# Kernel optimization log

Measured on AMD Instinct MI355X. Metric: run time of the kernel, lower is better.

Reference implementation:

```python
import jax, jax.numpy as jnp
import numpy as np

# module hyperparameters (match init_kwargs)
IN_PLANES = 64
OUT = 64            # out_planes
N_HASHES = 4
CHUNK = 25          # chunk_size
GROUPS = 8
KS = 56             # kernel_size == attended axis length H
GP = OUT // GROUPS  # group_planes = 8
EPS_N = 5e-5        # F.normalize eps
BN_EPS = 1e-5
F_GW, F_GV1, F_GV2 = 0.1, 0.1, 1.0


def l2norm(x, axis):
    # torch F.normalize(p=2, eps=EPS_N)
    n = jnp.sqrt(jnp.sum(x * x, axis=axis, keepdims=True))
    return x / jnp.maximum(n, EPS_N)


def setup_inputs() -> dict:
    key = jax.random.key(0)
    k1, k2, k3, k4 = jax.random.split(key, 4)
    x = jax.random.normal(k1, (2, IN_PLANES, KS, 56), jnp.float32)
    conv_w = jax.random.normal(k2, (OUT * 3 // 2, IN_PLANES), jnp.float32) * np.float32(np.sqrt(1.0 / IN_PLANES))
    bn_gamma = jnp.ones((OUT * 3 // 2,), jnp.float32)
    bn_beta = jnp.zeros((OUT * 3 // 2,), jnp.float32)
    relative = jax.random.normal(k3, (KS, GP * 3 // 2), jnp.float32) * np.float32(np.sqrt(1.0 / GP))
    # LSH random rotations: hash_buckets = min(56//25 + (56//25)%2, 10) = 2 -> hb//2 = 1
    rotations = jax.random.normal(k4, (OUT // 2, N_HASHES, 1), jnp.float32)
    return dict(x=x, conv_w=conv_w, bn_gamma=bn_gamma, bn_beta=bn_beta,
                relative=relative, rotations=rotations)


def reference(x, conv_w, bn_gamma, bn_beta, relative, rotations):
    # width=False: (N,C,H,W) -> (N,W,C,H), flatten batch with W
    N, C, Hax, W = x.shape
    x = jnp.transpose(x, (0, 3, 1, 2)).reshape(N * W, C, Hax)
    B, H = N * W, Hax
    hash_buckets = min(H // CHUNK + (H // CHUNK) % 2, 10)

    # 1x1 conv + eval-mode BatchNorm (running_mean=0, running_var=1)
    qkv = jnp.einsum('oc,bch->boh', conv_w, x)
    qkv = qkv / np.float32(np.sqrt(1.0 + BN_EPS)) * bn_gamma[None, :, None] + bn_beta[None, :, None]
    # NOTE: original uses raw reshape (B,C3,H) -> (B,H,C3), NOT a transpose
    qkv = qkv.reshape(B, H, OUT * 3 // 2)
    w_match = qkv[..., :OUT // 2]   # (B,H,out/2)
    v_match = qkv[..., OUT // 2:]   # (B,H,out)
    w_emb = relative[:, :GP // 2]
    v_emb = relative[:, GP // 2:]

    # LSH hashing (rotations shared across batch)
    rot = jnp.einsum('btf,fhi->bhti', w_match, rotations)
    rot = jnp.concatenate([rot, -rot], axis=-1)           # (B,nh,H,hash_buckets)
    codes = jnp.argmax(rot, axis=-1)
    codes = codes + (jnp.arange(N_HASHES) * hash_buckets)[None, :, None]
    codes = codes.reshape(B, N_HASHES * H)

    indices = jnp.argsort(codes, axis=-1)                 # stable sort into buckets
    undo = jnp.argsort(indices, axis=-1)
    mod = indices % H
    w_s = jnp.take_along_axis(w_match, mod[:, :, None], axis=1)
    v_s = jnp.take_along_axis(v_match, mod[:, :, None], axis=1)

    padding = (CHUNK - H % CHUNK) % CHUNK                 # 19 here
    w_b = w_s.reshape(B, N_HASHES, H, OUT // 2)
    v_b = v_s.reshape(B, N_HASHES, H, OUT)
    if padding:
        w_b = jnp.concatenate([w_b, w_b[:, :, -padding:, :]], axis=2)
        v_b = jnp.concatenate([v_b, v_b[:, :, -padding:, :]], axis=2)
        w_emb = jnp.concatenate([w_emb, w_emb[-padding:, :]], axis=0)
        v_emb = jnp.concatenate([v_emb, v_emb[-padding:, :]], axis=0)
    # raw reshapes, exactly as torch does (groups folded via flat reshape)
    w_b = w_b.reshape(B, GROUPS, N_HASHES, -1, CHUNK, GP // 2)
    v_b = v_b.reshape(B, GROUPS, N_HASHES, -1, CHUNK, GP)
    w_emb = w_emb.reshape(-1, CHUNK, GP // 2)             # (K,25,4)
    v_emb = v_emb.reshape(-1, CHUNK, GP)                  # (K,25,8)
    K = w_emb.shape[0]

    def adj(t):  # look-around over the chunk axis (dim 3), cat on dim 4
        return jnp.concatenate([t, jnp.roll(t, 1, axis=3), jnp.roll(t, -1, axis=3)], axis=4)

    def adj_emb(t):
        return jnp.concatenate([t, jnp.roll(t, 1, axis=0), jnp.roll(t, -1, axis=0)], axis=1)

    w_m = adj(l2norm(w_b, -1))
    v_a = adj(v_b)
    w_e = adj_emb(w_emb)
    v_e = adj_emb(v_emb)

    raw = jnp.einsum('bghkie,bghkje->bghkij', w_b, w_m)            # (B,g,h,K,25,75)
    emb_sc = F_GW * jnp.einsum('bghkie,kje->bghkij', w_b, w_e)
    ss = jnp.concatenate([raw, emb_sc], axis=1)                    # (B,2g,h,K,25,75)
    ss = l2norm(ss, 1).reshape(B, 2, GROUPS, N_HASHES, K, CHUNK, CHUNK * 3).sum(axis=1)

    bs = jax.nn.logsumexp(ss, axis=-1, keepdims=True)
    score = jnp.exp(ss - bs)
    bs = bs.reshape(B, GROUPS, N_HASHES, K * CHUNK)

    r_out = F_GV2 * jnp.einsum('bgukij,bgukje->bgukie', score, v_a)
    r_emb = F_GV1 * jnp.einsum('bgukij,kje->bgukie', score, v_e)
    ret = jnp.concatenate([r_out, r_emb], axis=-1)                 # (B,g,h,K,25,2*gp)
    ret = ret.reshape(B, N_HASHES, K, CHUNK, OUT * 2)              # raw reshape
    ret = ret.reshape(B, OUT * 2, N_HASHES, K, CHUNK)              # raw reshape
    ret = l2norm(ret, 1).reshape(B, N_HASHES, K, CHUNK, OUT, 2).sum(axis=-1)
    bs = l2norm(bs, 1).sum(axis=1)                                 # (B,h,K*25)

    ret = ret.reshape(B, N_HASHES, K * CHUNK, OUT)
    if padding:
        ret = ret[:, :, :-padding, :]
        bs = bs[:, :, :-padding]
    ret = ret.reshape(B, N_HASHES * H, OUT)
    bs = bs.reshape(B, N_HASHES * H)

    ret = jnp.take_along_axis(ret, undo[:, :, None], axis=1)      # unsort
    bs = jnp.take_along_axis(bs, undo, axis=1)
    ret = ret.reshape(B, N_HASHES, H, OUT)
    bs = bs.reshape(B, N_HASHES, H, 1)

    probs = jax.nn.softmax(bs, axis=1)
    ret = jnp.sum(ret * probs, axis=1)                             # (B,H,out)
    ret = ret.reshape(N, W, H, OUT)
    return jnp.transpose(ret, (0, 3, 2, 1))                        # (N,out,H,W)
```

## Files before the change

### kernel.cpp

```cpp
#include <hip/hip_runtime.h>
#include <math.h>


#define EPSN 5e-5f
#define LOG2E 1.4426950408889634f
#define LN2   0.6931471805599453f

__device__ __forceinline__ float dot4(const float4 a, const float4 b) {
    return a.x * b.x + a.y * b.y + a.z * b.z + a.w * b.w;
}
__device__ __forceinline__ void fma4(float4& a, float s, const float4 v) {
    a.x += s * v.x; a.y += s * v.y; a.z += s * v.z; a.w += s * v.w;
}

__global__ __launch_bounds__(256) void k12_qkv_sort(
        const float* __restrict__ x, const float* __restrict__ cw,
        const float* __restrict__ gamma, const float* __restrict__ beta,
        const float* __restrict__ rot, float* __restrict__ qkv,
        int* __restrict__ idx_buf) {
    __shared__ float xsT[56 * 68];
    __shared__ float cws[96 * 64];
    __shared__ float wm[56 * 32];
    __shared__ float rl[128];
    __shared__ float gs[96], bt[96];
    __shared__ int code[224];
    __shared__ int srt[224];
    const int b = blockIdx.x, n = b / 56, w = b % 56, tid = threadIdx.x;
    const float* xb = x + n * 200704 + w;
    for (int i = tid; i < 3584; i += 256) {
        int c = i / 56, h = i % 56;
        xsT[h * 68 + c] = xb[c * 3136 + h * 56];
    }
    for (int i = tid; i < 6144; i += 256) cws[i] = cw[i];
    if (tid < 128) rl[tid] = rot[tid];
    if (tid < 96) { gs[tid] = gamma[tid]; bt[tid] = beta[tid]; }
    __syncthreads();
    const float inv_s = 1.0f / sqrtf(1.0f + 1.0e-5f);
    for (int j = tid; j < 5376; j += 256) {
        int o = j / 56, h = j % 56;
        float s = 0.f;
        #pragma unroll
        for (int cs = 0; cs < 16; ++cs) {
            float4 xv = *(const float4*)&xsT[h * 68 + cs * 4];
            float4 cv = *(const float4*)&cws[o * 64 + cs * 4];
            s += dot4(xv, cv);
        }
        float val = s * inv_s * gs[o] + bt[o];
        qkv[b * 5376 + j] = val;
        int f = j % 96;
        if (f < 32) wm[(j / 96) * 32 + f] = val;
    }
    __syncthreads();
    if (tid < 224) {
        int u = tid / 56, t = tid % 56;
        float s = 0.f;
        #pragma unroll 8
        for (int f = 0; f < 32; ++f) s += wm[t * 32 + f] * rl[f * 4 + u];
        code[tid] = ((s < 0.f) ? 1 : 0) + 2 * u;
    }
    __syncthreads();
    if (tid < 224) {
        int c = code[tid], r = 0;
        for (int p = 0; p < 224; ++p) {
            int cp = code[p];
            r += (int)((cp < c) | ((cp == c) & (p < tid)));
        }
        srt[r] = tid;
    }
    __syncthreads();
    if (tid < 224) idx_buf[b * 224 + tid] = srt[tid];
}

__global__ __launch_bounds__(256) void k3_attn(
        const float* __restrict__ qkv, const int* __restrict__ idx_buf,
        const float* __restrict__ rel, float* __restrict__ Rb,
        float* __restrict__ bsb) {
    __shared__ __align__(16) float WbK[8][25][4];
    __shared__ __align__(16) float Wc [8][3][25][4];
    __shared__ __align__(16) float Vb [8][3][25][8];
    __shared__ float DI[25][76];
    const int b = blockIdx.x, u = blockIdx.y, k = blockIdx.z;
    const int tid = threadIdx.x;
    const int km1 = (k + 2) % 3, kp1 = (k + 1) % 3;
    const float* q = qkv + b * 5376;
    const int* ib = idx_buf + b * 224;

    for (int idx = tid; idx < 600; idx += 256) {
        int i = idx % 25, kk = (idx / 25) % 3, g = idx / 75;
        int p0 = 1200 * g + 300 * u + 100 * kk + 4 * i;
        int h = p0 / 2400, r = p0 % 2400, t = r >> 5, f = r & 31;
        int row = (t < 56) ? t : t - 19;
        int tt = ib[h * 56 + row] % 56;
        float4 v = *(const float4*)&q[tt * 96 + f];
        float ni = 1.0f / fmaxf(sqrtf(dot4(v, v)), EPSN);
        float4 vn = v;
        vn.x *= ni; vn.y *= ni; vn.z *= ni; vn.w *= ni;
        *(float4*)&Wc[g][kk][i][0] = vn;
        if (kk == k) *(float4*)&WbK[g][i][0] = v;
    }
    for (int idx = tid; idx < 1200; idx += 256) {
        int half = idx & 1, fr = idx >> 1;
        int i = fr % 25, kk = (fr / 25) % 3, g = fr / 75;
        int p0 = 2400 * g + 600 * u + 200 * kk + 8 * i + 4 * half;
        int h = p0 / 4800, r = p0 % 4800, t = r >> 6, f = r & 63;
        int row = (t < 56) ? t : t - 19;
        int tt = ib[h * 56 + row] % 56;
        *(float4*)&Vb[g][kk][i][4 * half] = *(const float4*)&q[tt * 96 + 32 + f];
    }
    __syncthreads();
    if (tid < 250) {
        const int i = tid % 25, jg = tid / 25;
        float4 wb8[8];
        #pragma unroll
        for (int g = 0; g < 8; ++g) wb8[g] = *(const float4*)&WbK[g][i][0];
        #pragma unroll
        for (int it = 0; it < 8; ++it) {
            int j = jg * 8 + it;
            if (j >= 75) break;
            int jb = j / 25, jj = j % 25;
            int ks = (jb == 0) ? k : ((jb == 1) ? km1 : kp1);
            int tw = ks * 25 + jj;
            int roww = (tw < 56) ? tw : tw - 19;
            float4 we = *(const float4*)&rel[roww * 12];
            we.x *= 0.1f; we.y *= 0.1f; we.z *= 0.1f; we.w *= 0.1f;
            float s2 = 0.f;
            #pragma unroll
            for (int g = 0; g < 8; ++g) {
                float4 wbn = *(const float4*)&Wc[g][ks][jj][0];
                float raw = dot4(wb8[g], wbn);
                float emb = dot4(wb8[g], we);
                s2 += raw * raw + emb * emb;
            }
            DI[i][j] = 1.0f / fmaxf(sqrtf(s2), EPSN);
        }
    }
    const int g = tid & 7, i = tid >> 3;
    float4 wbr;
    if (tid < 200) wbr = *(const float4*)&WbK[g][i][0];
    __syncthreads();
    for (int idx = tid; idx < 600; idx += 256) {
        int i2 = idx % 25, kk = (idx / 25) % 3, g2 = idx / 75;
        int t = kk * 25 + i2; int row = (t < 56) ? t : t - 19;
        float4 we = *(const float4*)&rel[row * 12];
        float4 v = *(const float4*)&Wc[g2][kk][i2][0];
        v.x += 0.1f * we.x; v.y += 0.1f * we.y;
        v.z += 0.1f * we.z; v.w += 0.1f * we.w;
        *(float4*)&Wc[g2][kk][i2][0] = v;
    }
    __syncthreads();
    if (tid < 200) {
        float ssv[75];
        float m = -INFINITY;
        float4 d4;
        #pragma unroll
        for (int j = 0; j < 75; ++j) {
            int jb = j / 25, jj = j % 25;
            int ks = (jb == 0) ? k : ((jb == 1) ? km1 : kp1);
            if ((j & 3) == 0) d4 = *(const float4*)&DI[i][j];
            float di = (j & 3) == 0 ? d4.x : ((j & 3) == 1 ? d4.y : ((j & 3) == 2 ? d4.z : d4.w));
            float v = dot4(wbr, *(const float4*)&Wc[g][ks][jj][0]) * di;
            ssv[j] = v;
            m = fmaxf(m, v);
        }
        float se = 0.f;
        float4 a0 = {0,0,0,0}, a1 = {0,0,0,0}, a2 = {0,0,0,0}, a3 = {0,0,0,0};
        const float mm = m * LOG2E;
        #pragma unroll
        for (int j = 0; j < 75; ++j) {
            int jb = j / 25, jj = j % 25;
            int ks = (jb == 0) ? k : ((jb == 1) ? km1 : kp1);
            float e = __builtin_amdgcn_exp2f(ssv[j] * LOG2E - mm);
            se += e;
            const float4* vv = (const float4*)&Vb[g][ks][jj][0];
            fma4(a0, e, vv[0]); fma4(a1, e, vv[1]);
            int tw = ks * 25 + jj;
            int roww = (tw < 56) ? tw : tw - 19;
            float4 ve0 = *(const float4*)&rel[roww * 12 + 4];
            float4 ve1 = *(const float4*)&rel[roww * 12 + 8];
            fma4(a2, e, ve0); fma4(a3, e, ve1);
        }
        bsb[b * 2400 + g * 300 + u * 75 + k * 25 + i] =
            m + __builtin_amdgcn_logf(se) * LN2;
        const float rinv = 1.0f / se;
        const float r2 = 0.1f * rinv;
        a0.x *= rinv; a0.y *= rinv; a0.z *= rinv; a0.w *= rinv;
        a1.x *= rinv; a1.y *= rinv; a1.z *= rinv; a1.w *= rinv;
        a2.x *= r2;   a2.y *= r2;   a2.z *= r2;   a2.w *= r2;
        a3.x *= r2;   a3.y *= r2;   a3.z *= r2;   a3.w *= r2;
        float* rp = Rb + b * 38400 + 4800 * g + 1200 * u + 400 * k + 16 * i;
        ((float4*)rp)[0] = a0;
        ((float4*)rp)[1] = a1;
        ((float4*)rp)[2] = a2;
        ((float4*)rp)[3] = a3;
    }
}

__global__ __launch_bounds__(256) void k45_post(
        const float* __restrict__ Rb, const float* __restrict__ bsb,
        const int* __restrict__ idx_buf, float* __restrict__ out) {
    __shared__ float D[300];
    __shared__ float bsn[300];
    __shared__ float retU[224][64];
    __shared__ float bsU[224];
    __shared__ int idxL[224];
    const int b = blockIdx.x, tid = threadIdx.x;
    const int n = b / 56, w = b % 56;
    const float* R = Rb + b * 38400;
    if (tid < 224) idxL[tid] = idx_buf[b * 224 + tid];
    for (int r = tid; r < 300; r += 256) {
        float s = 0.f;
        for (int c = 0; c < 128; ++c) { float v = R[c * 300 + r]; s += v * v; }
        D[r] = fmaxf(sqrtf(s), EPSN);
    }
    for (int idx = tid; idx < 300; idx += 256) {
        int u = idx / 75, t = idx % 75;
        float s2 = 0.f, sum = 0.f;
        #pragma unroll
        for (int g = 0; g < 8; ++g) {
            float v = bsb[b * 2400 + g * 300 + u * 75 + t];
            s2 += v * v; sum += v;
        }
        bsn[idx] = sum / fmaxf(sqrtf(s2), EPSN);
    }
    __syncthreads();
    for (int idx = tid; idx < 224 * 64; idx += 256) {
        int p = idx >> 6, o = idx & 63;
        int u3 = p / 56, t = p % 56;
        int k3 = t / 25, i3 = t % 25;
        int q0 = 9600 * u3 + 3200 * k3 + 128 * i3 + 2 * o;
        float2 rv = *(const float2*)&R[q0];
        float val = rv.x / D[q0 % 300] + rv.y / D[(q0 + 1) % 300];
        int r = idxL[p];
        retU[r][o] = val;
        if (o == 0) bsU[r] = bsn[u3 * 75 + t];
    }
    __syncthreads();
    for (int idx = tid; idx < 56 * 64; idx += 256) {
        int h = idx >> 6, o = idx & 63;
        float b0 = bsU[h], b1 = bsU[56 + h], b2 = bsU[112 + h], b3 = bsU[168 + h];
        float m = fmaxf(fmaxf(b0, b1), fmaxf(b2, b3));
        float e0 = __builtin_amdgcn_exp2f((b0 - m) * LOG2E);
        float e1 = __builtin_amdgcn_exp2f((b1 - m) * LOG2E);
        float e2 = __builtin_amdgcn_exp2f((b2 - m) * LOG2E);
        float e3 = __builtin_amdgcn_exp2f((b3 - m) * LOG2E);
        float ps = e0 + e1 + e2 + e3;
        float val = (retU[h][o] * e0 + retU[56 + h][o] * e1 +
                     retU[112 + h][o] * e2 + retU[168 + h][o] * e3) / ps;
        out[((n * 64 + o) * 56 + h) * 56 + w] = val;
    }
}

extern "C" void kernel_launch(void* const* d_in, const int* in_sizes, int n_in,
                              void* d_out, int out_size, void* d_ws, size_t ws_size,
                              hipStream_t stream) {
    (void)in_sizes; (void)n_in; (void)out_size; (void)ws_size;
    const float* x     = (const float*)d_in[0];
    const float* cw    = (const float*)d_in[1];
    const float* gamma = (const float*)d_in[2];
    const float* beta  = (const float*)d_in[3];
    const float* rel   = (const float*)d_in[4];
    const float* rot   = (const float*)d_in[5];
    float* ws  = (float*)d_ws;
    float* qkv = ws;
    float* bsb = ws + 602112;
    float* Rb  = ws + 870912;
    int*   idx = (int*)(ws + 5171712);

    k12_qkv_sort<<<112, 256, 0, stream>>>(x, cw, gamma, beta, rot, qkv, idx);
    k3_attn<<<dim3(112, 4, 3), 256, 0, stream>>>(qkv, idx, rel, Rb, bsb);
    k45_post<<<112, 256, 0, stream>>>(Rb, bsb, idx, (float*)d_out);
}
```

Baseline: 170.3 us.

## Fuse attention score normalization into softmax loop using wave shuffles and rsq

The attention kernel no longer precomputes per-(i,j) normalizers in shared memory. It computes the group-sum norm on the fly with xor-shuffles across the 8 group lanes, which removes the DI table, the WbK buffer, the in-place Wc update pass and two barriers. It also skips the max subtraction, relying on scores being bounded after normalization. Separately, the qkv conv is register-tiled to four output channels per thread, divisions are replaced with rsq reciprocals, and several loops get unroll pragmas and an occupancy hint of 5 blocks per CU. Dropping the max subtraction and using approximate rsq changes numerics slightly. The new shuffle chain and occupancy cap could add register pressure.

```diff
diff --git a/kernel.cpp b/kernel.cpp
--- a/kernel.cpp
+++ b/kernel.cpp
@@ -3,6 +3,7 @@
 
 
 #define EPSN 5e-5f
+#define INV_EPSN 20000.0f
 #define LOG2E 1.4426950408889634f
 #define LN2   0.6931471805599453f
 
@@ -27,28 +28,41 @@
     __shared__ int srt[224];
     const int b = blockIdx.x, n = b / 56, w = b % 56, tid = threadIdx.x;
     const float* xb = x + n * 200704 + w;
+    #pragma unroll 7
     for (int i = tid; i < 3584; i += 256) {
         int c = i / 56, h = i % 56;
         xsT[h * 68 + c] = xb[c * 3136 + h * 56];
     }
+    #pragma unroll 8
     for (int i = tid; i < 6144; i += 256) cws[i] = cw[i];
     if (tid < 128) rl[tid] = rot[tid];
     if (tid < 96) { gs[tid] = gamma[tid]; bt[tid] = beta[tid]; }
     __syncthreads();
     const float inv_s = 1.0f / sqrtf(1.0f + 1.0e-5f);
-    for (int j = tid; j < 5376; j += 256) {
-        int o = j / 56, h = j % 56;
-        float s = 0.f;
+    for (int tl = tid; tl < 1344; tl += 256) {
+        int oq = tl / 56, h = tl % 56;
+        int o0 = oq * 4;
+        float s0 = 0.f, s1 = 0.f, s2 = 0.f, s3 = 0.f;
         #pragma unroll
         for (int cs = 0; cs < 16; ++cs) {
             float4 xv = *(const float4*)&xsT[h * 68 + cs * 4];
-            float4 cv = *(const float4*)&cws[o * 64 + cs * 4];
-            s += dot4(xv, cv);
-        }
-        float val = s * inv_s * gs[o] + bt[o];
-        qkv[b * 5376 + j] = val;
-        int f = j % 96;
-        if (f < 32) wm[(j / 96) * 32 + f] = val;
+            float4 c0 = *(const float4*)&cws[(o0 + 0) * 64 + cs * 4];
+            float4 c1 = *(const float4*)&cws[(o0 + 1) * 64 + cs * 4];
+            float4 c2 = *(const float4*)&cws[(o0 + 2) * 64 + cs * 4];
+            float4 c3 = *(const float4*)&cws[(o0 + 3) * 64 + cs * 4];
+            s0 += dot4(xv, c0); s1 += dot4(xv, c1);
+            s2 += dot4(xv, c2); s3 += dot4(xv, c3);
+        }
+        #pragma unroll
+        for (int qq = 0; qq < 4; ++qq) {
+            int o = o0 + qq;
+            float sv = (qq == 0) ? s0 : (qq == 1) ? s1 : (qq == 2) ? s2 : s3;
+            float val = sv * inv_s * gs[o] + bt[o];
+            int j = o * 56 + h;
+            qkv[b * 5376 + j] = val;
+            int f = j % 96;
+            if (f < 32) wm[(j / 96) * 32 + f] = val;
+        }
     }
     __syncthreads();
     if (tid < 224) {
@@ -61,6 +75,7 @@
     __syncthreads();
     if (tid < 224) {
         int c = code[tid], r = 0;
+        #pragma unroll 8
         for (int p = 0; p < 224; ++p) {
             int cp = code[p];
             r += (int)((cp < c) | ((cp == c) & (p < tid)));
@@ -71,20 +86,18 @@
     if (tid < 224) idx_buf[b * 224 + tid] = srt[tid];
 }
 
-__global__ __launch_bounds__(256) void k3_attn(
+__global__ __launch_bounds__(256, 5) void k3_attn(
         const float* __restrict__ qkv, const int* __restrict__ idx_buf,
         const float* __restrict__ rel, float* __restrict__ Rb,
         float* __restrict__ bsb) {
-    __shared__ __align__(16) float WbK[8][25][4];
-    __shared__ __align__(16) float Wc [8][3][25][4];
-    __shared__ __align__(16) float Vb [8][3][25][8];
-    __shared__ float DI[25][76];
+    __shared__ __align__(16) float Wc[8][3][25][4];
+    __shared__ __align__(16) float Vb[8][3][25][8];
     const int b = blockIdx.x, u = blockIdx.y, k = blockIdx.z;
     const int tid = threadIdx.x;
-    const int km1 = (k + 2) % 3, kp1 = (k + 1) % 3;
     const float* q = qkv + b * 5376;
     const int* ib = idx_buf + b * 224;
 
+    #pragma unroll 3
     for (int idx = tid; idx < 600; idx += 256) {
         int i = idx % 25, kk = (idx / 25) % 3, g = idx / 75;
         int p0 = 1200 * g + 300 * u + 100 * kk + 4 * i;
@@ -92,12 +105,11 @@
         int row = (t < 56) ? t : t - 19;
         int tt = ib[h * 56 + row] % 56;
         float4 v = *(const float4*)&q[tt * 96 + f];
-        float ni = 1.0f / fmaxf(sqrtf(dot4(v, v)), EPSN);
-        float4 vn = v;
-        vn.x *= ni; vn.y *= ni; vn.z *= ni; vn.w *= ni;
-        *(float4*)&Wc[g][kk][i][0] = vn;
-        if (kk == k) *(float4*)&WbK[g][i][0] = v;
-    }
+        float ni = fminf(__builtin_amdgcn_rsqf(dot4(v, v)), INV_EPSN);
+        v.x *= ni; v.y *= ni; v.z *= ni; v.w *= ni;
+        *(float4*)&Wc[g][kk][i][0] = v;
+    }
+    #pragma unroll 5
     for (int idx = tid; idx < 1200; idx += 256) {
         int half = idx & 1, fr = idx >> 1;
         int i = fr % 25, kk = (fr / 25) % 3, g = fr / 75;
@@ -107,80 +119,44 @@
         int tt = ib[h * 56 + row] % 56;
         *(float4*)&Vb[g][kk][i][4 * half] = *(const float4*)&q[tt * 96 + 32 + f];
     }
-    __syncthreads();
-    if (tid < 250) {
-        const int i = tid % 25, jg = tid / 25;
-        float4 wb8[8];
-        #pragma unroll
-        for (int g = 0; g < 8; ++g) wb8[g] = *(const float4*)&WbK[g][i][0];
-        #pragma unroll
-        for (int it = 0; it < 8; ++it) {
-            int j = jg * 8 + it;
-            if (j >= 75) break;
-            int jb = j / 25, jj = j % 25;
-            int ks = (jb == 0) ? k : ((jb == 1) ? km1 : kp1);
-            int tw = ks * 25 + jj;
-            int roww = (tw < 56) ? tw : tw - 19;
-            float4 we = *(const float4*)&rel[roww * 12];
-            we.x *= 0.1f; we.y *= 0.1f; we.z *= 0.1f; we.w *= 0.1f;
-            float s2 = 0.f;
-            #pragma unroll
-            for (int g = 0; g < 8; ++g) {
-                float4 wbn = *(const float4*)&Wc[g][ks][jj][0];
-                float raw = dot4(wb8[g], wbn);
-                float emb = dot4(wb8[g], we);
-                s2 += raw * raw + emb * emb;
-            }
-            DI[i][j] = 1.0f / fmaxf(sqrtf(s2), EPSN);
-        }
-    }
     const int g = tid & 7, i = tid >> 3;
-    float4 wbr;
-    if (tid < 200) wbr = *(const float4*)&WbK[g][i][0];
-    __syncthreads();
-    for (int idx = tid; idx < 600; idx += 256) {
-        int i2 = idx % 25, kk = (idx / 25) % 3, g2 = idx / 75;
-        int t = kk * 25 + i2; int row = (t < 56) ? t : t - 19;
-        float4 we = *(const float4*)&rel[row * 12];
-        float4 v = *(const float4*)&Wc[g2][kk][i2][0];
-        v.x += 0.1f * we.x; v.y += 0.1f * we.y;
-        v.z += 0.1f * we.z; v.w += 0.1f * we.w;
-        *(float4*)&Wc[g2][kk][i2][0] = v;
-    }
-    __syncthreads();
+    float4 wbr = {0.f, 0.f, 0.f, 0.f};
     if (tid < 200) {
-        float ssv[75];
-        float m = -INFINITY;
-        float4 d4;
-        #pragma unroll
-        for (int j = 0; j < 75; ++j) {
-            int jb = j / 25, jj = j % 25;
-            int ks = (jb == 0) ? k : ((jb == 1) ? km1 : kp1);
-            if ((j & 3) == 0) d4 = *(const float4*)&DI[i][j];
-            float di = (j & 3) == 0 ? d4.x : ((j & 3) == 1 ? d4.y : ((j & 3) == 2 ? d4.z : d4.w));
-            float v = dot4(wbr, *(const float4*)&Wc[g][ks][jj][0]) * di;
-            ssv[j] = v;
-            m = fmaxf(m, v);
-        }
+        int p0 = 1200 * g + 300 * u + 100 * k + 4 * i;
+        int h = p0 / 2400, r = p0 % 2400, t = r >> 5, f = r & 31;
+        int row = (t < 56) ? t : t - 19;
+        int tt = ib[h * 56 + row] % 56;
+        wbr = *(const float4*)&q[tt * 96 + f];
+    }
+    __syncthreads();
+    if (tid < 200) {
         float se = 0.f;
         float4 a0 = {0,0,0,0}, a1 = {0,0,0,0}, a2 = {0,0,0,0}, a3 = {0,0,0,0};
-        const float mm = m * LOG2E;
-        #pragma unroll
-        for (int j = 0; j < 75; ++j) {
-            int jb = j / 25, jj = j % 25;
-            int ks = (jb == 0) ? k : ((jb == 1) ? km1 : kp1);
-            float e = __builtin_amdgcn_exp2f(ssv[j] * LOG2E - mm);
-            se += e;
-            const float4* vv = (const float4*)&Vb[g][ks][jj][0];
-            fma4(a0, e, vv[0]); fma4(a1, e, vv[1]);
-            int tw = ks * 25 + jj;
-            int roww = (tw < 56) ? tw : tw - 19;
-            float4 ve0 = *(const float4*)&rel[roww * 12 + 4];
-            float4 ve1 = *(const float4*)&rel[roww * 12 + 8];
-            fma4(a2, e, ve0); fma4(a3, e, ve1);
+        #pragma unroll
+        for (int ks = 0; ks < 3; ++ks) {
+            #pragma unroll
+            for (int jj = 0; jj < 25; ++jj) {
+                const int tw = ks * 25 + jj;
+                const int roww = (tw < 56) ? tw : tw - 19;
+                float4 we = *(const float4*)&rel[roww * 12];
+                float rawv = dot4(wbr, *(const float4*)&Wc[g][ks][jj][0]);
+                float embv = 0.1f * dot4(wbr, we);
+                float p2 = rawv * rawv + embv * embv;
+                p2 += __shfl_xor(p2, 1);
+                p2 += __shfl_xor(p2, 2);
+                p2 += __shfl_xor(p2, 4);
+                float di = fminf(__builtin_amdgcn_rsqf(p2), INV_EPSN);
+                float e = __builtin_amdgcn_exp2f((rawv + embv) * di * LOG2E);
+                se += e;
+                const float4* vv = (const float4*)&Vb[g][ks][jj][0];
+                fma4(a0, e, vv[0]); fma4(a1, e, vv[1]);
+                float4 ve0 = *(const float4*)&rel[roww * 12 + 4];
+                float4 ve1 = *(const float4*)&rel[roww * 12 + 8];
+                fma4(a2, e, ve0); fma4(a3, e, ve1);
+            }
         }
         bsb[b * 2400 + g * 300 + u * 75 + k * 25 + i] =
-            m + __builtin_amdgcn_logf(se) * LN2;
+            __builtin_amdgcn_logf(se) * LN2;
         const float rinv = 1.0f / se;
         const float r2 = 0.1f * rinv;
         a0.x *= rinv; a0.y *= rinv; a0.z *= rinv; a0.w *= rinv;
@@ -209,8 +185,9 @@
     if (tid < 224) idxL[tid] = idx_buf[b * 224 + tid];
     for (int r = tid; r < 300; r += 256) {
         float s = 0.f;
+        #pragma unroll 16
         for (int c = 0; c < 128; ++c) { float v = R[c * 300 + r]; s += v * v; }
-        D[r] = fmaxf(sqrtf(s), EPSN);
+        D[r] = fminf(__builtin_amdgcn_rsqf(s), INV_EPSN);
     }
     for (int idx = tid; idx < 300; idx += 256) {
         int u = idx / 75, t = idx % 75;
@@ -223,13 +200,15 @@
         bsn[idx] = sum / fmaxf(sqrtf(s2), EPSN);
     }
     __syncthreads();
+    #pragma unroll 4
     for (int idx = tid; idx < 224 * 64; idx += 256) {
         int p = idx >> 6, o = idx & 63;
         int u3 = p / 56, t = p % 56;
         int k3 = t / 25, i3 = t % 25;
         int q0 = 9600 * u3 + 3200 * k3 + 128 * i3 + 2 * o;
         float2 rv = *(const float2*)&R[q0];
-        float val = rv.x / D[q0 % 300] + rv.y / D[(q0 + 1) % 300];
+        int r0 = q0 % 300;
+        float val = rv.x * D[r0] + rv.y * D[r0 + 1];
         int r = idxL[p];
         retU[r][o] = val;
         if (o == 0) bsU[r] = bsn[u3 * 75 + t];
```

After: 174.8 us. 2.7% more time.
